# Kernel optimization log

Measured on AMD Instinct MI355X. Metric: run time of the kernel, lower is better.

Reference implementation:

```python
import jax, jax.numpy as jnp
import numpy as np

SCALE_EXP = 1.0
DIM = 64      # per-head dim
HEADS = 16
C = 1.5 - SCALE_EXP  # = 0.5

B, L, D_IN = 4, 2048, 1024


def setup_inputs() -> dict:
    key = jax.random.key(0)
    k1, k2, k3 = jax.random.split(key, 3)
    x = jax.random.normal(k1, (B, L, D_IN), dtype=jnp.float32)
    # kernel_init for qk: normal(stddev = dim**(c-0.5)) = dim**0 = 1 for scale_exp=1
    Wqk = jax.random.normal(k2, (D_IN, 2 * HEADS * DIM), dtype=jnp.float32) * (DIM ** (C - 0.5))
    bqk = jnp.zeros((2 * HEADS * DIM,), dtype=jnp.float32)
    Wv = jax.random.normal(k3, (D_IN, HEADS * DIM), dtype=jnp.float32)  # stddev 1.0
    bv = jnp.zeros((HEADS * DIM,), dtype=jnp.float32)
    return {"x": x, "Wqk": Wqk, "bqk": bqk, "Wv": Wv, "bv": bv}


def reference(x, Wqk, bqk, Wv, bv):
    d_in = x.shape[-1]
    # qk projection, scaled by d_in**c
    qk = (x @ Wqk + bqk) / (d_in ** C)            # [b, l, 2*h*d]
    b, l, _ = qk.shape
    qk = qk.reshape(b, l, HEADS, 2 * DIM).transpose(0, 2, 1, 3)  # [b, h, l, 2d]
    q, k = jnp.split(qk, 2, axis=-1)              # each [b, h, l, d]
    v = (x @ Wv + bv) / jnp.sqrt(jnp.asarray(d_in, x.dtype))
    v = v.reshape(b, l, HEADS, DIM).transpose(0, 2, 1, 3)        # [b, h, l, d]
    A = (1.0 / (DIM ** SCALE_EXP)) * jnp.einsum('bhqd,bhkd->bhqk', q, k)
    phi_A = jax.nn.softmax(A, axis=-1)
    out = jnp.einsum('bhqk,bhkd->bhqd', phi_A, v)                # [b, h, l, d]
    return out.transpose(0, 2, 1, 3).reshape(b, l, HEADS * DIM)  # [b, l, h*d]
```

## Files before the change

### kernel.cpp

```cpp
#include <hip/hip_runtime.h>
#include <hip/hip_bf16.h>

typedef __attribute__((ext_vector_type(8))) short bf16x8;
typedef __attribute__((ext_vector_type(4))) float f32x4;
typedef __hip_bfloat16 bf16;

#define MFMA_16x16x32(a, b, c) __builtin_amdgcn_mfma_f32_16x16x32_bf16((a), (b), (c), 0, 0, 0)

#define ASM_VMCNT4()  asm volatile("s_waitcnt vmcnt(4)" ::: "memory")
#define ASM_VMCNT0()  asm volatile("s_waitcnt vmcnt(0)" ::: "memory")
#define ASM_BARRIER() asm volatile("s_waitcnt lgkmcnt(0)\n\ts_barrier" ::: "memory")

typedef __attribute__((address_space(1))) void as1_void;
typedef __attribute__((address_space(3))) void as3_void;

__device__ __forceinline__ void g2lds16(const void* g, void* l) {
  __builtin_amdgcn_global_load_lds((as1_void*)(void*)g, (as3_void*)l, 16, 0, 0);
}

__global__ __launch_bounds__(256) void cast_x(const float* __restrict__ src,
                                              bf16* __restrict__ dst, int n8, float scale) {
  int i = blockIdx.x * 256 + threadIdx.x;
  if (i >= n8) return;
  const float4* s4 = (const float4*)src;
  float4 f0 = s4[i * 2], f1 = s4[i * 2 + 1];
  float vals[8] = {f0.x, f0.y, f0.z, f0.w, f1.x, f1.y, f1.z, f1.w};
  union { unsigned short u[8]; uint4 v; } o;
#pragma unroll
  for (int j = 0; j < 8; ++j) {
    bf16 hv = __float2bfloat16(vals[j] * scale);
    o.u[j] = *(unsigned short*)&hv;
  }
  ((uint4*)dst)[i] = o.v;
}

__global__ __launch_bounds__(256) void transpose_cast(const float* __restrict__ src,
                                                      bf16* __restrict__ dst, int K, int N) {
  __shared__ float tile[32][33];
  int n0 = blockIdx.x * 32, k0 = blockIdx.y * 32;
  int tx = threadIdx.x, ty = threadIdx.y;
#pragma unroll
  for (int i = 0; i < 4; ++i) {
    int kl = i * 8 + ty;
    tile[kl][tx] = src[(size_t)(k0 + kl) * N + n0 + tx];
  }
  __syncthreads();
#pragma unroll
  for (int i = 0; i < 4; ++i) {
    int nl = i * 8 + ty;
    dst[(size_t)(n0 + nl) * K + k0 + tx] = __float2bfloat16(tile[tx][nl]);
  }
}

__global__ __launch_bounds__(256) void proj_gemm(
    const bf16* __restrict__ A, const bf16* __restrict__ Bt,
    const float* __restrict__ bqk, const float* __restrict__ bv,
    bf16* __restrict__ Qb, bf16* __restrict__ Kb, bf16* __restrict__ Vtb) {
  __shared__ __align__(16) bf16 As[128 * 32];
  __shared__ __align__(16) bf16 Bs[128 * 32];
  const int tid = threadIdx.x, lane = tid & 63, w = tid >> 6;
  const int wm = w >> 1, wn = w & 1;
  const int l15 = lane & 15, g = lane >> 4;
  const int m0 = blockIdx.x * 128, n0 = blockIdx.y * 128;

  f32x4 acc[4][4];
#pragma unroll
  for (int i = 0; i < 4; ++i)
#pragma unroll
    for (int j = 0; j < 4; ++j) acc[i][j] = (f32x4)0.f;

  const bf16* ap[2];
  const bf16* bp[2];
  unsigned off[2];
#pragma unroll
  for (int i = 0; i < 2; ++i) {
    int s = i * 256 + tid;
    int row = s >> 2, pos = s & 3;
    int kp = ((pos ^ ((row >> 1) & 3)) << 3);
    ap[i] = A + (size_t)(m0 + row) * 1024 + kp;
    bp[i] = Bt + (size_t)(n0 + row) * 1024 + kp;
    off[i] = (i * 256 + w * 64) * 8;
  }

  const int swc = (l15 >> 1) & 3;

  for (int kt = 0; kt < 32; ++kt) {
    if (kt) ASM_BARRIER();
#pragma unroll
    for (int i = 0; i < 2; ++i) {
      g2lds16(ap[i], &As[off[i]]);
      g2lds16(bp[i], &Bs[off[i]]);
      ap[i] += 32;
      bp[i] += 32;
    }
    ASM_VMCNT0();
    ASM_BARRIER();

    bf16x8 af[4], bfr[4];
#pragma unroll
    for (int f = 0; f < 4; ++f) {
      af[f]  = *(const bf16x8*)&As[(wm * 64 + f * 16 + l15) * 32 + ((g ^ swc) << 3)];
      bfr[f] = *(const bf16x8*)&Bs[(wn * 64 + f * 16 + l15) * 32 + ((g ^ swc) << 3)];
    }
    __builtin_amdgcn_s_setprio(1);
#pragma unroll
    for (int fm = 0; fm < 4; ++fm)
#pragma unroll
      for (int fn = 0; fn < 4; ++fn)
        acc[fm][fn] = MFMA_16x16x32(af[fm], bfr[fn], acc[fm][fn]);
    __builtin_amdgcn_s_setprio(0);
  }

  const float INV32 = 1.f / 32.f;
  const float QSCALE = 0.125f * 1.44269504088896340736f;
#pragma unroll
  for (int fm = 0; fm < 4; ++fm) {
#pragma unroll
    for (int fn = 0; fn < 4; ++fn) {
      int n = n0 + wn * 64 + fn * 16 + l15;
#pragma unroll
      for (int r = 0; r < 4; ++r) {
        int m = m0 + wm * 64 + fm * 16 + 4 * g + r;
        int b = m >> 11, lrow = m & 2047;
        float val = acc[fm][fn][r];
        if (n < 2048) {
          float vb = val + bqk[n] * INV32;
          int h = n >> 7, wi = n & 127;
          if (wi < 64) Qb[(((size_t)b * 16 + h) * 2048 + lrow) * 64 + wi] = __float2bfloat16(vb * QSCALE);
          else         Kb[(((size_t)b * 16 + h) * 2048 + lrow) * 64 + (wi - 64)] = __float2bfloat16(vb * 0.125f);
        } else {
          int nv = n - 2048;
          val = val + bv[nv] * INV32;
          int h = nv >> 6, d = nv & 63;
          Vtb[(((size_t)b * 16 + h) * 64 + d) * 2048 + lrow] = __float2bfloat16(val);
        }
      }
    }
  }
}

__global__ __launch_bounds__(256) void attn(
    const bf16* __restrict__ Qb, const bf16* __restrict__ Kb,
    const bf16* __restrict__ Vtb, float* __restrict__ out) {
  __shared__ __align__(16) bf16 Ks[2][64 * 64];
  __shared__ __align__(16) bf16 Vs[2][64 * 64];

  const int bh = blockIdx.x;
  const int qt = blockIdx.y;
  const int b = bh >> 4, h = bh & 15;
  const int tid = threadIdx.x, lane = tid & 63, w = tid >> 6;
  const int l15 = lane & 15, g = lane >> 4;

  const bf16* Kbh = Kb + (size_t)bh * 2048 * 64;
  const bf16* Vbh = Vtb + (size_t)bh * 64 * 2048;

  const bf16* qbase = Qb + ((size_t)bh * 2048 + qt * 128 + w * 32) * 64;
  bf16x8 qa[2][2];
#pragma unroll
  for (int qc = 0; qc < 2; ++qc)
#pragma unroll
    for (int ks = 0; ks < 2; ++ks)
      qa[qc][ks] = *(const bf16x8*)(qbase + (qc * 16 + l15) * 64 + ks * 32 + g * 8);

  bf16x8 aone;
#pragma unroll
  for (int j = 0; j < 8; ++j) aone[j] = (l15 == 0) ? (short)0x3F80 : (short)0;

  f32x4 acc[2][5];
#pragma unroll
  for (int qc = 0; qc < 2; ++qc)
#pragma unroll
    for (int da = 0; da < 5; ++da) acc[qc][da] = (f32x4)0.f;

  const bf16* kp[2];
  const bf16* vp[2];
  unsigned ldsoff[2];
#pragma unroll
  for (int i = 0; i < 2; ++i) {
    int s = (w * 2 + i) * 64 + lane;
    int row = s >> 3, blk = s & 7;
    int swk = (row & 3) | ((row & 8) >> 1);
    kp[i] = Kbh + (size_t)row * 64 + ((blk ^ swk) << 3);
    vp[i] = Vbh + (size_t)row * 2048 + ((blk ^ (row & 7)) << 3);
    ldsoff[i] = (w * 2 + i) * 512;
  }

  auto stage = [&](int bufi) {
#pragma unroll
    for (int i = 0; i < 2; ++i) {
      g2lds16(kp[i], &Ks[bufi][ldsoff[i]]);
      g2lds16(vp[i], &Vs[bufi][ldsoff[i]]);
      kp[i] += 64 * 64;
      vp[i] += 64;
    }
  };

  stage(0);
  int cur = 0;
  const f32x4 z4 = (f32x4)0.f;

  for (int t = 0; t < 32; ++t) {
    if (t < 31) { stage(cur ^ 1); ASM_VMCNT4(); }
    else        { ASM_VMCNT0(); }
    ASM_BARRIER();

    f32x4 s_acc[2][4];
    __builtin_amdgcn_s_setprio(1);
#pragma unroll
    for (int kb = 0; kb < 4; ++kb) {
      const int krow = ((kb & 2) << 4) + ((l15 >> 2) << 3) + ((kb & 1) << 2) + (l15 & 3);
      const int swk = (krow & 3) | ((krow & 8) >> 1);
      bf16x8 ak0 = *(const bf16x8*)&Ks[cur][krow * 64 + ((g ^ swk) << 3)];
      bf16x8 ak1 = *(const bf16x8*)&Ks[cur][krow * 64 + (((4 + g) ^ swk) << 3)];
      s_acc[0][kb] = MFMA_16x16x32(ak1, qa[0][1], MFMA_16x16x32(ak0, qa[0][0], z4));
      s_acc[1][kb] = MFMA_16x16x32(ak1, qa[1][1], MFMA_16x16x32(ak0, qa[1][0], z4));
    }
    __builtin_amdgcn_s_setprio(0);

    bf16x8 pb[2][2];
#pragma unroll
    for (int qc = 0; qc < 2; ++qc) {
#pragma unroll
      for (int ks = 0; ks < 2; ++ks) {
        union { unsigned int u[4]; bf16x8 v; } pk;
#pragma unroll
        for (int u = 0; u < 4; ++u) {
          const int kbp = 2 * ks + (u >> 1);
          const int r0 = (2 * u) & 3;
          float lo = __builtin_amdgcn_exp2f(s_acc[qc][kbp][r0]);
          float hi = __builtin_amdgcn_exp2f(s_acc[qc][kbp][r0 + 1]);
          __hip_bfloat162 h2 = __float22bfloat162_rn(float2{lo, hi});
          pk.u[u] = *(unsigned int*)&h2;
        }
        pb[qc][ks] = pk.v;
      }
    }

    __builtin_amdgcn_s_setprio(1);
#pragma unroll
    for (int ks = 0; ks < 2; ++ks) {
#pragma unroll
      for (int da = 0; da < 4; ++da) {
        const int vrow = da * 16 + l15;
        bf16x8 av = *(const bf16x8*)&Vs[cur][vrow * 64 + (((ks * 4 + g) ^ (l15 & 7)) << 3)];
        acc[0][da] = MFMA_16x16x32(av, pb[0][ks], acc[0][da]);
        acc[1][da] = MFMA_16x16x32(av, pb[1][ks], acc[1][da]);
      }
      acc[0][4] = MFMA_16x16x32(aone, pb[0][ks], acc[0][4]);
      acc[1][4] = MFMA_16x16x32(aone, pb[1][ks], acc[1][4]);
    }
    __builtin_amdgcn_s_setprio(0);

    if (t < 31) ASM_BARRIER();
    cur ^= 1;
  }

#pragma unroll
  for (int qc = 0; qc < 2; ++qc) {
    const float lsum = __shfl(acc[qc][4][0], l15, 64);
    const float inv = 1.f / lsum;
    const int lrow = qt * 128 + w * 32 + qc * 16 + l15;
    float* orow = out + ((size_t)b * 2048 + lrow) * 1024 + h * 64 + 4 * g;
#pragma unroll
    for (int da = 0; da < 4; ++da) {
      float4 o4 = {acc[qc][da][0] * inv, acc[qc][da][1] * inv,
                   acc[qc][da][2] * inv, acc[qc][da][3] * inv};
      *(float4*)(orow + da * 16) = o4;
    }
  }
}

extern "C" void kernel_launch(void* const* d_in, const int* in_sizes, int n_in,
                              void* d_out, int out_size, void* d_ws, size_t ws_size,
                              hipStream_t stream) {
  (void)in_sizes; (void)n_in; (void)out_size; (void)ws_size;
  const float* x   = (const float*)d_in[0];
  const float* Wqk = (const float*)d_in[1];
  const float* bqk = (const float*)d_in[2];
  const float* Wv  = (const float*)d_in[3];
  const float* bv  = (const float*)d_in[4];
  float* outp = (float*)d_out;

  char* ws = (char*)d_ws;
  bf16* xb  = (bf16*)(ws);
  bf16* Wt  = (bf16*)(ws + 16777216);
  bf16* Qb  = (bf16*)(ws + 23068672);
  bf16* Kb  = (bf16*)(ws + 39845888);
  bf16* Vtb = (bf16*)(ws + 56623104);

  cast_x<<<4096, 256, 0, stream>>>(x, xb, 1048576, 1.f / 32.f);
  transpose_cast<<<dim3(64, 32), dim3(32, 8), 0, stream>>>(Wqk, Wt, 1024, 2048);
  transpose_cast<<<dim3(32, 32), dim3(32, 8), 0, stream>>>(Wv, Wt + (size_t)2048 * 1024, 1024, 1024);
  proj_gemm<<<dim3(64, 24), 256, 0, stream>>>(xb, Wt, bqk, bv, Qb, Kb, Vtb);
  attn<<<dim3(64, 16), 256, 0, stream>>>(Qb, Kb, Vtb, outp);
}
```

Before: 193.2 us.

## Double-buffer projection GEMM with 128x256 tiles, BK=64 and interleaved prefetch

Restructures the QKV projection GEMM to use 512-thread blocks computing 128x256 output tiles. The K step grows to 64 and the LDS buffers are double-buffered with an 8-way XOR swizzle. Global-to-LDS prefetch of the next K tile is split into phases interleaved with four MFMA sub-steps, so memory latency overlaps compute instead of stalling at a vmcnt(0) every iteration. This adds many barriers and more LDS per block, which may reduce occupancy or add sync overhead. The epilogue still indexes n with wn*64, so it must stay consistent with the 4-wide wn layout.

```diff
diff --git a/kernel.cpp b/kernel.cpp
--- a/kernel.cpp
+++ b/kernel.cpp
@@ -10,6 +10,8 @@
 #define ASM_VMCNT4()  asm volatile("s_waitcnt vmcnt(4)" ::: "memory")
 #define ASM_VMCNT0()  asm volatile("s_waitcnt vmcnt(0)" ::: "memory")
 #define ASM_BARRIER() asm volatile("s_waitcnt lgkmcnt(0)\n\ts_barrier" ::: "memory")
+#define ASM_SBAR()    asm volatile("s_barrier" ::: "memory")
+#define ASM_LGKM0()   asm volatile("s_waitcnt lgkmcnt(0)" ::: "memory")
 
 typedef __attribute__((address_space(1))) void as1_void;
 typedef __attribute__((address_space(3))) void as3_void;
@@ -52,16 +54,17 @@
   }
 }
 
-__global__ __launch_bounds__(256) void proj_gemm(
+__global__ __launch_bounds__(512, 2) void proj_gemm(
     const bf16* __restrict__ A, const bf16* __restrict__ Bt,
     const float* __restrict__ bqk, const float* __restrict__ bv,
     bf16* __restrict__ Qb, bf16* __restrict__ Kb, bf16* __restrict__ Vtb) {
-  __shared__ __align__(16) bf16 As[128 * 32];
-  __shared__ __align__(16) bf16 Bs[128 * 32];
+  __shared__ __align__(16) bf16 As[2][128 * 64];
+  __shared__ __align__(16) bf16 Bs[2][256 * 64];
   const int tid = threadIdx.x, lane = tid & 63, w = tid >> 6;
-  const int wm = w >> 1, wn = w & 1;
+  const int wm = w >> 2, wn = w & 3;
   const int l15 = lane & 15, g = lane >> 4;
-  const int m0 = blockIdx.x * 128, n0 = blockIdx.y * 128;
+  const int m0 = blockIdx.x * 128, n0 = blockIdx.y * 256;
+  const int swz = l15 & 7;
 
   f32x4 acc[4][4];
 #pragma unroll
@@ -70,45 +73,96 @@
     for (int j = 0; j < 4; ++j) acc[i][j] = (f32x4)0.f;
 
   const bf16* ap[2];
-  const bf16* bp[2];
-  unsigned off[2];
+  unsigned offA[2];
 #pragma unroll
   for (int i = 0; i < 2; ++i) {
-    int s = i * 256 + tid;
-    int row = s >> 2, pos = s & 3;
-    int kp = ((pos ^ ((row >> 1) & 3)) << 3);
-    ap[i] = A + (size_t)(m0 + row) * 1024 + kp;
-    bp[i] = Bt + (size_t)(n0 + row) * 1024 + kp;
-    off[i] = (i * 256 + w * 64) * 8;
-  }
-
-  const int swc = (l15 >> 1) & 3;
-
-  for (int kt = 0; kt < 32; ++kt) {
-    if (kt) ASM_BARRIER();
-#pragma unroll
-    for (int i = 0; i < 2; ++i) {
-      g2lds16(ap[i], &As[off[i]]);
-      g2lds16(bp[i], &Bs[off[i]]);
-      ap[i] += 32;
-      bp[i] += 32;
-    }
-    ASM_VMCNT0();
-    ASM_BARRIER();
-
-    bf16x8 af[4], bfr[4];
-#pragma unroll
-    for (int f = 0; f < 4; ++f) {
-      af[f]  = *(const bf16x8*)&As[(wm * 64 + f * 16 + l15) * 32 + ((g ^ swc) << 3)];
-      bfr[f] = *(const bf16x8*)&Bs[(wn * 64 + f * 16 + l15) * 32 + ((g ^ swc) << 3)];
-    }
+    int s = i * 512 + tid, r = s >> 3, c = s & 7;
+    ap[i] = A + (size_t)(m0 + r) * 1024 + ((c ^ (r & 7)) << 3);
+    offA[i] = (unsigned)s * 8;
+  }
+  const bf16* bp[4];
+  unsigned offB[4];
+#pragma unroll
+  for (int i = 0; i < 4; ++i) {
+    int s = i * 512 + tid, r = s >> 3, c = s & 7;
+    bp[i] = Bt + (size_t)(n0 + r) * 1024 + ((c ^ (r & 7)) << 3);
+    offB[i] = (unsigned)s * 8;
+  }
+
+  auto stageP0 = [&](int bufi) {
+#pragma unroll
+    for (int i = 0; i < 2; ++i) { g2lds16(ap[i], &As[bufi][offA[i]]); ap[i] += 64; }
+#pragma unroll
+    for (int i = 0; i < 2; ++i) { g2lds16(bp[i], &Bs[bufi][offB[i]]); bp[i] += 64; }
+  };
+  auto stageP1 = [&](int bufi) {
+#pragma unroll
+    for (int i = 2; i < 4; ++i) { g2lds16(bp[i], &Bs[bufi][offB[i]]); bp[i] += 64; }
+  };
+
+  stageP0(0);
+  stageP1(0);
+  ASM_VMCNT0();
+  ASM_SBAR();
+
+  for (int kt = 0; kt < 16; ++kt) {
+    const bf16* Ac = &As[kt & 1][0];
+    const bf16* Bc = &Bs[kt & 1][0];
+    const int nb = (kt & 1) ^ 1;
+    const bool pre = (kt < 15);
+
+    bf16x8 af[2][4], bq[2];
+#pragma unroll
+    for (int ks = 0; ks < 2; ++ks)
+#pragma unroll
+      for (int fm = 0; fm < 4; ++fm)
+        af[ks][fm] = *(const bf16x8*)&Ac[(wm * 64 + fm * 16 + l15) * 64 + (((ks * 4 + g) ^ swz) << 3)];
+#pragma unroll
+    for (int ks = 0; ks < 2; ++ks)
+      bq[ks] = *(const bf16x8*)&Bc[(wn * 64 + 0 * 16 + l15) * 64 + (((ks * 4 + g) ^ swz) << 3)];
+    if (pre) stageP0(nb);
+    ASM_SBAR(); ASM_LGKM0();
     __builtin_amdgcn_s_setprio(1);
 #pragma unroll
     for (int fm = 0; fm < 4; ++fm)
-#pragma unroll
-      for (int fn = 0; fn < 4; ++fn)
-        acc[fm][fn] = MFMA_16x16x32(af[fm], bfr[fn], acc[fm][fn]);
-    __builtin_amdgcn_s_setprio(0);
+      acc[fm][0] = MFMA_16x16x32(af[1][fm], bq[1], MFMA_16x16x32(af[0][fm], bq[0], acc[fm][0]));
+    __builtin_amdgcn_s_setprio(0);
+    ASM_SBAR();
+
+#pragma unroll
+    for (int ks = 0; ks < 2; ++ks)
+      bq[ks] = *(const bf16x8*)&Bc[(wn * 64 + 1 * 16 + l15) * 64 + (((ks * 4 + g) ^ swz) << 3)];
+    if (pre) stageP1(nb);
+    ASM_SBAR(); ASM_LGKM0();
+    __builtin_amdgcn_s_setprio(1);
+#pragma unroll
+    for (int fm = 0; fm < 4; ++fm)
+      acc[fm][1] = MFMA_16x16x32(af[1][fm], bq[1], MFMA_16x16x32(af[0][fm], bq[0], acc[fm][1]));
+    __builtin_amdgcn_s_setprio(0);
+    ASM_SBAR();
+
+#pragma unroll
+    for (int ks = 0; ks < 2; ++ks)
+      bq[ks] = *(const bf16x8*)&Bc[(wn * 64 + 2 * 16 + l15) * 64 + (((ks * 4 + g) ^ swz) << 3)];
+    ASM_SBAR(); ASM_LGKM0();
+    __builtin_amdgcn_s_setprio(1);
+#pragma unroll
+    for (int fm = 0; fm < 4; ++fm)
+      acc[fm][2] = MFMA_16x16x32(af[1][fm], bq[1], MFMA_16x16x32(af[0][fm], bq[0], acc[fm][2]));
+    __builtin_amdgcn_s_setprio(0);
+    ASM_SBAR();
+
+#pragma unroll
+    for (int ks = 0; ks < 2; ++ks)
+      bq[ks] = *(const bf16x8*)&Bc[(wn * 64 + 3 * 16 + l15) * 64 + (((ks * 4 + g) ^ swz) << 3)];
+    if (pre) ASM_VMCNT0();
+    ASM_SBAR(); ASM_LGKM0();
+    __builtin_amdgcn_s_setprio(1);
+#pragma unroll
+    for (int fm = 0; fm < 4; ++fm)
+      acc[fm][3] = MFMA_16x16x32(af[1][fm], bq[1], MFMA_16x16x32(af[0][fm], bq[0], acc[fm][3]));
+    __builtin_amdgcn_s_setprio(0);
+    ASM_SBAR();
   }
 
   const float INV32 = 1.f / 32.f;
@@ -291,6 +345,6 @@
   cast_x<<<4096, 256, 0, stream>>>(x, xb, 1048576, 1.f / 32.f);
   transpose_cast<<<dim3(64, 32), dim3(32, 8), 0, stream>>>(Wqk, Wt, 1024, 2048);
   transpose_cast<<<dim3(32, 32), dim3(32, 8), 0, stream>>>(Wv, Wt + (size_t)2048 * 1024, 1024, 1024);
-  proj_gemm<<<dim3(64, 24), 256, 0, stream>>>(xb, Wt, bqk, bv, Qb, Kb, Vtb);
+  proj_gemm<<<dim3(64, 12), 512, 0, stream>>>(xb, Wt, bqk, bv, Qb, Kb, Vtb);
   attn<<<dim3(64, 16), 256, 0, stream>>>(Qb, Kb, Vtb, outp);
 }
```

After: 207.5 us. 7.4% more time.
